# Kernel optimization log

Measured on AMD Instinct MI355X. Metric: run time of the kernel, lower is better.

The kernel has to match this reference:

```python
import jax, jax.numpy as jnp
import numpy as np

EMBEDDING_DIM = 128
METRIC_MARGIN = 1.0
EPS = 1e-8


def setup_inputs() -> dict:
    key = jax.random.key(0)
    X = jax.random.normal(key, (8192, EMBEDDING_DIM), dtype=jnp.float32)
    return {"X": X}


def reference(X):
    B, d = X.shape
    P = B // 2  # number of positive pairs (2p, 2p+1)
    # Pairwise similarity matrix (original uses broadcasted mul+sum; this is the GEMM form)
    D = (X @ X.T) / d  # [B, B]
    E = jnp.exp(D + METRIC_MARGIN)  # [B, B]

    # For pair p: sum of exp over rows 2p and 2p+1, excluding columns {2p, 2p+1}
    pair_row_sum = E.sum(axis=1).reshape(P, 2).sum(axis=1)  # [P]
    # 2x2 diagonal blocks E[2p:2p+2, 2p:2p+2]
    blocks = jnp.einsum('pipj->pij', E.reshape(P, 2, P, 2))  # [P, 2, 2]
    S = pair_row_sum - blocks.sum(axis=(1, 2))  # [P]

    even = jnp.arange(0, B, 2)
    D_pos = D[even, even + 1]  # D[2p, 2p+1], [P]

    J = jnp.log(EPS + S) - D_pos  # [P]
    loss = jnp.mean(jnp.maximum(J, 0.0) ** 2) / 2.0
    return loss
```

## Files before the change

kernel.cpp:

```cpp
#include <hip/hip_runtime.h>
#include <hip/hip_bf16.h>

#define NROWS 8192
#define DIM   128
#define NPAIR (NROWS / 2)
#define CSPLIT 16
#define COLS_PER_CS (NROWS / CSPLIT)
#define CTILE 128
#define TILES_PER_CS (COLS_PER_CS / CTILE)
#define MREP 2
#define ROWS_PER_BLOCK 128

typedef __attribute__((ext_vector_type(8))) short bf16x8;
typedef __attribute__((ext_vector_type(4))) float f32x4;

__device__ inline float exp2_fast(float x) {
#if __has_builtin(__builtin_amdgcn_exp2f)
    return __builtin_amdgcn_exp2f(x);
#else
    return exp2f(x);
#endif
}

__device__ inline unsigned short f2bf(float f) {
    unsigned int u = __float_as_uint(f);
    unsigned int r = (u + 0x7fffu + ((u >> 16) & 1u)) >> 16;
    return (unsigned short)r;
}

#define SCL_F 0.0112710550069450f
#define L2E_F 1.4426950408889634f

__global__ __launch_bounds__(256) void k_convert(const float* __restrict__ X,
                                                 unsigned short* __restrict__ Xc) {
    int id = blockIdx.x * 256 + threadIdx.x;
    float4 v = reinterpret_cast<const float4*>(X)[id];
    ushort4 o;
    o.x = f2bf(v.x); o.y = f2bf(v.y); o.z = f2bf(v.z); o.w = f2bf(v.w);
    reinterpret_cast<ushort4*>(Xc)[id] = o;
}

__global__ __launch_bounds__(256) void k_rowsum(const unsigned short* __restrict__ Xc,
                                                float* __restrict__ partial) {
    __shared__ unsigned short Bt[CTILE * DIM];
    const int tid  = threadIdx.x;
    const int wave = tid >> 6;
    const int lane = tid & 63;
    const int l15  = lane & 15;
    const int lhi  = lane >> 4;
    const int rowbase = blockIdx.x * ROWS_PER_BLOCK + wave * (MREP * 16);
    const int cs = blockIdx.y;

    bf16x8 a00, a01, a02, a03, a10, a11, a12, a13;
    {
        const unsigned short* r0 = Xc + (size_t)(rowbase + l15) * DIM + lhi * 8;
        const unsigned short* r1 = r0 + 16 * DIM;
        a00 = *reinterpret_cast<const bf16x8*>(r0);
        a01 = *reinterpret_cast<const bf16x8*>(r0 + 32);
        a02 = *reinterpret_cast<const bf16x8*>(r0 + 64);
        a03 = *reinterpret_cast<const bf16x8*>(r0 + 96);
        a10 = *reinterpret_cast<const bf16x8*>(r1);
        a11 = *reinterpret_cast<const bf16x8*>(r1 + 32);
        a12 = *reinterpret_cast<const bf16x8*>(r1 + 64);
        a13 = *reinterpret_cast<const bf16x8*>(r1 + 96);
    }
    asm volatile("" : "+v"(a00), "+v"(a01), "+v"(a02), "+v"(a03));
    asm volatile("" : "+v"(a10), "+v"(a11), "+v"(a12), "+v"(a13));

    f32x4 esum0 = {0.f, 0.f, 0.f, 0.f};
    f32x4 esum1 = {0.f, 0.f, 0.f, 0.f};

    for (int it = 0; it < TILES_PER_CS; ++it) {
        const int c0 = cs * COLS_PER_CS + it * CTILE;

#pragma unroll 2
        for (int j = 0; j < 8; ++j) {
            int d   = j * 256 + tid;
            int col = d >> 4;
            int seg = d & 15;
            bf16x8 v = *reinterpret_cast<const bf16x8*>(
                Xc + (size_t)(c0 + col) * DIM + seg * 8);
            *reinterpret_cast<bf16x8*>(
                &Bt[(((size_t)col << 4) | (seg ^ (col & 7))) * 8]) = v;
        }
        __syncthreads();

        for (int ct = 0; ct < CTILE / 16; ++ct) {
            const int c = ct * 16 + l15;
            const int x = c & 7;
            const unsigned short* lb = &Bt[(size_t)c * DIM];
            bf16x8 b0 = *reinterpret_cast<const bf16x8*>(lb + (((lhi     ) ^ x) * 8));
            bf16x8 b1 = *reinterpret_cast<const bf16x8*>(lb + (((lhi + 4 ) ^ x) * 8));
            bf16x8 b2 = *reinterpret_cast<const bf16x8*>(lb + (((lhi + 8 ) ^ x) * 8));
            bf16x8 b3 = *reinterpret_cast<const bf16x8*>(lb + (((lhi + 12) ^ x) * 8));

            f32x4 d0 = {0.f, 0.f, 0.f, 0.f};
            f32x4 d1 = {0.f, 0.f, 0.f, 0.f};
            d0 = __builtin_amdgcn_mfma_f32_16x16x32_bf16(a00, b0, d0, 0, 0, 0);
            d1 = __builtin_amdgcn_mfma_f32_16x16x32_bf16(a10, b0, d1, 0, 0, 0);
            d0 = __builtin_amdgcn_mfma_f32_16x16x32_bf16(a01, b1, d0, 0, 0, 0);
            d1 = __builtin_amdgcn_mfma_f32_16x16x32_bf16(a11, b1, d1, 0, 0, 0);
            d0 = __builtin_amdgcn_mfma_f32_16x16x32_bf16(a02, b2, d0, 0, 0, 0);
            d1 = __builtin_amdgcn_mfma_f32_16x16x32_bf16(a12, b2, d1, 0, 0, 0);
            d0 = __builtin_amdgcn_mfma_f32_16x16x32_bf16(a03, b3, d0, 0, 0, 0);
            d1 = __builtin_amdgcn_mfma_f32_16x16x32_bf16(a13, b3, d1, 0, 0, 0);

            esum0[0] += exp2_fast(fmaf(d0[0], SCL_F, L2E_F));
            esum0[1] += exp2_fast(fmaf(d0[1], SCL_F, L2E_F));
            esum0[2] += exp2_fast(fmaf(d0[2], SCL_F, L2E_F));
            esum0[3] += exp2_fast(fmaf(d0[3], SCL_F, L2E_F));
            esum1[0] += exp2_fast(fmaf(d1[0], SCL_F, L2E_F));
            esum1[1] += exp2_fast(fmaf(d1[1], SCL_F, L2E_F));
            esum1[2] += exp2_fast(fmaf(d1[2], SCL_F, L2E_F));
            esum1[3] += exp2_fast(fmaf(d1[3], SCL_F, L2E_F));
        }
        __syncthreads();
    }

#pragma unroll
    for (int m = 0; m < MREP; ++m) {
#pragma unroll
        for (int j = 0; j < 4; ++j) {
            float v = (m == 0) ? esum0[j] : esum1[j];
            v += __shfl_xor(v, 1, 64);
            v += __shfl_xor(v, 2, 64);
            v += __shfl_xor(v, 4, 64);
            v += __shfl_xor(v, 8, 64);
            if (l15 == 0) {
                int row = rowbase + m * 16 + lhi * 4 + j;
                partial[(size_t)row * CSPLIT + cs] = v;
            }
        }
    }
}

__global__ __launch_bounds__(256) void k_loss1(const float* __restrict__ X,
                                               const float* __restrict__ partial,
                                               float* __restrict__ lpart) {
    int p = blockIdx.x * 256 + threadIdx.x;
    const float4* a = reinterpret_cast<const float4*>(X + (size_t)(2 * p) * DIM);
    const float4* b = reinterpret_cast<const float4*>(X + (size_t)(2 * p + 1) * DIM);
    float d00 = 0.f, d01 = 0.f, d11 = 0.f;
#pragma unroll 8
    for (int i = 0; i < DIM / 4; ++i) {
        float4 av = a[i], bv = b[i];
        d00 += av.x * av.x + av.y * av.y + av.z * av.z + av.w * av.w;
        d01 += av.x * bv.x + av.y * bv.y + av.z * bv.z + av.w * bv.w;
        d11 += bv.x * bv.x + bv.y * bv.y + bv.z * bv.z + bv.w * bv.w;
    }
    float D01 = d01 * (1.0f / DIM);
    float blocksum = __expf(d00 * (1.0f / DIM) + 1.0f)
                   + 2.0f * __expf(D01 + 1.0f)
                   + __expf(d11 * (1.0f / DIM) + 1.0f);

    const float4* pp = reinterpret_cast<const float4*>(partial + (size_t)(2 * p) * CSPLIT);
    float S = 0.0f;
#pragma unroll
    for (int i = 0; i < 2 * CSPLIT / 4; ++i) {
        float4 v = pp[i];
        S += v.x + v.y + v.z + v.w;
    }
    S -= blocksum;
    float J = logf(1e-8f + S) - D01;
    float t = fmaxf(J, 0.0f);
    float acc = t * t;

    __shared__ float red[4];
    float v = acc;
#pragma unroll
    for (int off = 32; off >= 1; off >>= 1) v += __shfl_down(v, off, 64);
    if ((threadIdx.x & 63) == 0) red[threadIdx.x >> 6] = v;
    __syncthreads();
    if (threadIdx.x == 0)
        lpart[blockIdx.x] = red[0] + red[1] + red[2] + red[3];
}

__global__ __launch_bounds__(64) void k_final(const float* __restrict__ lpart,
                                              float* __restrict__ out) {
    float v = (threadIdx.x < 16) ? lpart[threadIdx.x] : 0.0f;
#pragma unroll
    for (int off = 8; off >= 1; off >>= 1) v += __shfl_down(v, off, 64);
    if (threadIdx.x == 0) out[0] = v * (1.0f / (2.0f * NPAIR));
}

extern "C" void kernel_launch(void* const* d_in, const int* in_sizes, int n_in,
                              void* d_out, int out_size, void* d_ws, size_t ws_size,
                              hipStream_t stream) {
    const float* X = (const float*)d_in[0];
    float* out = (float*)d_out;

    unsigned short* Xc = (unsigned short*)d_ws;
    float* partial = (float*)(Xc + (size_t)NROWS * DIM);
    float* lpart = partial + (size_t)NROWS * CSPLIT;

    k_convert<<<dim3((NROWS * DIM / 4) / 256), dim3(256), 0, stream>>>(X, Xc);
    k_rowsum<<<dim3(NROWS / ROWS_PER_BLOCK, CSPLIT), dim3(256), 0, stream>>>(Xc, partial);
    k_loss1<<<dim3(NPAIR / 256), dim3(256), 0, stream>>>(X, partial, lpart);
    k_final<<<dim3(1), dim3(64), 0, stream>>>(lpart, out);
}
```

Measured before the change: 47.94 us.

## Prefetch next column tile into registers and fold exp scaling into A operand

The row-sum kernel now loads the next 64-column tile from global memory into registers while the current tile is being computed, and drops the trailing barrier in exchange for a smaller tile. The conversion kernel also writes a second, pre-scaled bf16 copy of X for the A operand, so the exp argument no longer needs a per-element FMA; the constant e factor is applied once per row at the end. Launch bounds now request 4 blocks per SM to raise occupancy. The risks are the extra bf16 copy written by the conversion kernel and the rounding error of scaling before bf16 conversion.

```diff
diff --git a/kernel.cpp b/kernel.cpp
--- a/kernel.cpp
+++ b/kernel.cpp
@@ -6,8 +6,8 @@
 #define NPAIR (NROWS / 2)
 #define CSPLIT 16
 #define COLS_PER_CS (NROWS / CSPLIT)
-#define CTILE 128
-#define TILES_PER_CS (COLS_PER_CS / CTILE)
+#define CTILE 64
+#define NT (COLS_PER_CS / CTILE)
 #define MREP 2
 #define ROWS_PER_BLOCK 128
 
@@ -29,19 +29,24 @@
 }
 
 #define SCL_F 0.0112710550069450f
-#define L2E_F 1.4426950408889634f
+#define E1_F  2.7182818284590452f
 
 __global__ __launch_bounds__(256) void k_convert(const float* __restrict__ X,
+                                                 unsigned short* __restrict__ Xa,
                                                  unsigned short* __restrict__ Xc) {
     int id = blockIdx.x * 256 + threadIdx.x;
     float4 v = reinterpret_cast<const float4*>(X)[id];
-    ushort4 o;
-    o.x = f2bf(v.x); o.y = f2bf(v.y); o.z = f2bf(v.z); o.w = f2bf(v.w);
-    reinterpret_cast<ushort4*>(Xc)[id] = o;
-}
-
-__global__ __launch_bounds__(256) void k_rowsum(const unsigned short* __restrict__ Xc,
-                                                float* __restrict__ partial) {
+    ushort4 oa, oc;
+    oa.x = f2bf(v.x * SCL_F); oa.y = f2bf(v.y * SCL_F);
+    oa.z = f2bf(v.z * SCL_F); oa.w = f2bf(v.w * SCL_F);
+    oc.x = f2bf(v.x); oc.y = f2bf(v.y); oc.z = f2bf(v.z); oc.w = f2bf(v.w);
+    reinterpret_cast<ushort4*>(Xa)[id] = oa;
+    reinterpret_cast<ushort4*>(Xc)[id] = oc;
+}
+
+__global__ __launch_bounds__(256, 4) void k_rowsum(const unsigned short* __restrict__ Xa,
+                                                   const unsigned short* __restrict__ Xc,
+                                                   float* __restrict__ partial) {
     __shared__ unsigned short Bt[CTILE * DIM];
     const int tid  = threadIdx.x;
     const int wave = tid >> 6;
@@ -53,7 +58,7 @@
 
     bf16x8 a00, a01, a02, a03, a10, a11, a12, a13;
     {
-        const unsigned short* r0 = Xc + (size_t)(rowbase + l15) * DIM + lhi * 8;
+        const unsigned short* r0 = Xa + (size_t)(rowbase + l15) * DIM + lhi * 8;
         const unsigned short* r1 = r0 + 16 * DIM;
         a00 = *reinterpret_cast<const bf16x8*>(r0);
         a01 = *reinterpret_cast<const bf16x8*>(r0 + 32);
@@ -70,26 +75,38 @@
     f32x4 esum0 = {0.f, 0.f, 0.f, 0.f};
     f32x4 esum1 = {0.f, 0.f, 0.f, 0.f};
 
-    for (int it = 0; it < TILES_PER_CS; ++it) {
-        const int c0 = cs * COLS_PER_CS + it * CTILE;
-
-#pragma unroll 2
-        for (int j = 0; j < 8; ++j) {
-            int d   = j * 256 + tid;
-            int col = d >> 4;
-            int seg = d & 15;
-            bf16x8 v = *reinterpret_cast<const bf16x8*>(
-                Xc + (size_t)(c0 + col) * DIM + seg * 8);
-            *reinterpret_cast<bf16x8*>(
-                &Bt[(((size_t)col << 4) | (seg ^ (col & 7))) * 8]) = v;
+    const int tcol = tid >> 4;
+    const int tseg = tid & 15;
+    const unsigned short* gsrc = Xc + (size_t)(cs * COLS_PER_CS + tcol) * DIM + tseg * 8;
+    const int lslot = (tcol << 4) | (tseg ^ (tcol & 7));
+
+    bf16x8 st0, st1, st2, st3;
+    st0 = *reinterpret_cast<const bf16x8*>(gsrc);
+    st1 = *reinterpret_cast<const bf16x8*>(gsrc + 16 * DIM);
+    st2 = *reinterpret_cast<const bf16x8*>(gsrc + 32 * DIM);
+    st3 = *reinterpret_cast<const bf16x8*>(gsrc + 48 * DIM);
+
+    for (int it = 0; it < NT; ++it) {
+        if (it) __syncthreads();
+        *reinterpret_cast<bf16x8*>(&Bt[(size_t)(lslot      ) * 8]) = st0;
+        *reinterpret_cast<bf16x8*>(&Bt[(size_t)(lslot + 256) * 8]) = st1;
+        *reinterpret_cast<bf16x8*>(&Bt[(size_t)(lslot + 512) * 8]) = st2;
+        *reinterpret_cast<bf16x8*>(&Bt[(size_t)(lslot + 768) * 8]) = st3;
+        __syncthreads();
+
+        if (it + 1 < NT) {
+            const unsigned short* nb = gsrc + (size_t)(it + 1) * CTILE * DIM;
+            st0 = *reinterpret_cast<const bf16x8*>(nb);
+            st1 = *reinterpret_cast<const bf16x8*>(nb + 16 * DIM);
+            st2 = *reinterpret_cast<const bf16x8*>(nb + 32 * DIM);
+            st3 = *reinterpret_cast<const bf16x8*>(nb + 48 * DIM);
         }
-        __syncthreads();
-
+
+        const int x = l15 & 7;
+#pragma unroll
         for (int ct = 0; ct < CTILE / 16; ++ct) {
-            const int c = ct * 16 + l15;
-            const int x = c & 7;
-            const unsigned short* lb = &Bt[(size_t)c * DIM];
-            bf16x8 b0 = *reinterpret_cast<const bf16x8*>(lb + (((lhi     ) ^ x) * 8));
+            const unsigned short* lb = &Bt[(size_t)(ct * 16 + l15) * DIM];
+            bf16x8 b0 = *reinterpret_cast<const bf16x8*>(lb + ((lhi      ^ x) * 8));
             bf16x8 b1 = *reinterpret_cast<const bf16x8*>(lb + (((lhi + 4 ) ^ x) * 8));
             bf16x8 b2 = *reinterpret_cast<const bf16x8*>(lb + (((lhi + 8 ) ^ x) * 8));
             bf16x8 b3 = *reinterpret_cast<const bf16x8*>(lb + (((lhi + 12) ^ x) * 8));
@@ -105,16 +122,11 @@
             d0 = __builtin_amdgcn_mfma_f32_16x16x32_bf16(a03, b3, d0, 0, 0, 0);
             d1 = __builtin_amdgcn_mfma_f32_16x16x32_bf16(a13, b3, d1, 0, 0, 0);
 
-            esum0[0] += exp2_fast(fmaf(d0[0], SCL_F, L2E_F));
-            esum0[1] += exp2_fast(fmaf(d0[1], SCL_F, L2E_F));
-            esum0[2] += exp2_fast(fmaf(d0[2], SCL_F, L2E_F));
-            esum0[3] += exp2_fast(fmaf(d0[3], SCL_F, L2E_F));
-            esum1[0] += exp2_fast(fmaf(d1[0], SCL_F, L2E_F));
-            esum1[1] += exp2_fast(fmaf(d1[1], SCL_F, L2E_F));
-            esum1[2] += exp2_fast(fmaf(d1[2], SCL_F, L2E_F));
-            esum1[3] += exp2_fast(fmaf(d1[3], SCL_F, L2E_F));
+            esum0[0] += exp2_fast(d0[0]); esum0[1] += exp2_fast(d0[1]);
+            esum0[2] += exp2_fast(d0[2]); esum0[3] += exp2_fast(d0[3]);
+            esum1[0] += exp2_fast(d1[0]); esum1[1] += exp2_fast(d1[1]);
+            esum1[2] += exp2_fast(d1[2]); esum1[3] += exp2_fast(d1[3]);
         }
-        __syncthreads();
     }
 
 #pragma unroll
@@ -128,7 +140,7 @@
             v += __shfl_xor(v, 8, 64);
             if (l15 == 0) {
                 int row = rowbase + m * 16 + lhi * 4 + j;
-                partial[(size_t)row * CSPLIT + cs] = v;
+                partial[(size_t)row * CSPLIT + cs] = v * E1_F;
             }
         }
     }
@@ -189,12 +201,13 @@
     const float* X = (const float*)d_in[0];
     float* out = (float*)d_out;
 
-    unsigned short* Xc = (unsigned short*)d_ws;
+    unsigned short* Xa = (unsigned short*)d_ws;
+    unsigned short* Xc = Xa + (size_t)NROWS * DIM;
     float* partial = (float*)(Xc + (size_t)NROWS * DIM);
     float* lpart = partial + (size_t)NROWS * CSPLIT;
 
-    k_convert<<<dim3((NROWS * DIM / 4) / 256), dim3(256), 0, stream>>>(X, Xc);
-    k_rowsum<<<dim3(NROWS / ROWS_PER_BLOCK, CSPLIT), dim3(256), 0, stream>>>(Xc, partial);
+    k_convert<<<dim3((NROWS * DIM / 4) / 256), dim3(256), 0, stream>>>(X, Xa, Xc);
+    k_rowsum<<<dim3(NROWS / ROWS_PER_BLOCK, CSPLIT), dim3(256), 0, stream>>>(Xa, Xc, partial);
     k_loss1<<<dim3(NPAIR / 256), dim3(256), 0, stream>>>(X, partial, lpart);
     k_final<<<dim3(1), dim3(64), 0, stream>>>(lpart, out);
 }
```

Result: faster. 41.39 us (median of 2 runs) (-13.7%).
